# Performance work log

Hardware: AMD Instinct MI355X
Metric: run time of the kernel (lower is better)

## Reference

```python
import jax, jax.numpy as jnp
import numpy as np

K = 4
TEMPERATURE = 34.0
OUT_CH = 256
KSIZE = 3
PAD = 1


def setup_inputs() -> dict:
    key = jax.random.key(0)
    ks = jax.random.split(key, 6)
    B, C, H, W = 16, 256, 56, 56
    hidden = int(C * 0.25) + 1  # 65
    x = jax.random.normal(ks[0], (B, C, H, W), dtype=jnp.float32)
    w_fc1 = jax.random.normal(ks[1], (hidden, C), dtype=jnp.float32) * (2.0 / C) ** 0.5
    w_fc2 = jax.random.normal(ks[2], (K, hidden), dtype=jnp.float32) * (2.0 / hidden) ** 0.5
    b_fc2 = jnp.zeros((K,), dtype=jnp.float32)
    weight = jax.random.normal(ks[3], (OUT_CH, C, KSIZE, KSIZE), dtype=jnp.float32) * 0.05
    bias = jax.random.normal(ks[4], (K, OUT_CH), dtype=jnp.float32) * 0.01
    return {"x": x, "w_fc1": w_fc1, "w_fc2": w_fc2, "b_fc2": b_fc2,
            "weight": weight, "bias": bias}


def _attention(x, w_fc1, w_fc2, b_fc2):
    pooled = x.mean(axis=(2, 3))                     # [B, C] adaptive avgpool(1)
    h = jax.nn.relu(pooled @ w_fc1.T)                # 1x1 conv == linear
    raw = h @ w_fc2.T + b_fc2                        # [B, K]
    # gradient_approximation: hard one-hot fwd, softmax(x/T) bwd (straight-through)
    hard = jax.nn.one_hot(jnp.argmax(raw, axis=1), raw.shape[1], dtype=raw.dtype)
    soft = jax.nn.softmax(raw / TEMPERATURE, axis=1)
    att = jax.lax.stop_gradient(hard - soft) + soft
    return att, raw


def _quantize_banks(weight):
    # WDoReFaQuantizer with 'modified' scheme, bits 2..K+1, STE on the round step
    w = weight.reshape(-1)
    t = jnp.tanh(w)
    xq = t / jnp.max(jnp.abs(t))
    xq = (xq + 1.0) * 0.5                            # in [0, 1]
    banks = []
    for bit in range(2, 2 + K):
        a = float(1 << bit)
        q = jnp.minimum(jnp.floor(a * xq), a - 1.0) / a
        q = jax.lax.stop_gradient(q - xq) + xq       # STE: identity backward
        banks.append(q * 2.0 - 1.0)
    return jnp.stack(banks)                          # [K, O*C*k*k]


def reference(x, w_fc1, w_fc2, b_fc2, weight, bias):
    B, C, H, W = x.shape
    att, raw = _attention(x, w_fc1, w_fc2, b_fc2)    # [B, K], [B, K]
    wq = _quantize_banks(weight)                     # [K, N]
    agg_w = (att @ wq).reshape(B, OUT_CH, C, KSIZE, KSIZE)
    agg_b = att @ bias                               # [B, OUT_CH]

    def conv1(xi, wi):  # xi: [C,H,W], wi: [O,C,k,k]
        return jax.lax.conv_general_dilated(
            xi[None], wi, window_strides=(1, 1),
            padding=[(PAD, PAD), (PAD, PAD)],
            dimension_numbers=("NCHW", "OIHW", "NCHW"))[0]

    out = jax.vmap(conv1)(x, agg_w) + agg_b[:, :, None, None]
    return (out, raw)
```

## Files before the change

kernel.cpp:

```cpp
#include <hip/hip_runtime.h>
#include <math.h>

#define NB 16
#define NC 256
#define NH 56
#define NW 56
#define NHW 3136
#define NHID 65
#define NK 4
#define NOC 256
#define WN 589824
#define OUT0 12845056

#define WS_POOLED 0
#define WS_KB     4096
#define WS_MAX    4112
#define WS_MAXP   4128
#define WS_WQF    8192
#define WQB_OFF   32768ul
#define XP_OFF    4751360ul
#define WS_NEED   32325632ul

typedef unsigned int u32;
typedef unsigned short u16;
typedef unsigned long long u64;
typedef __attribute__((ext_vector_type(8))) short s8v;
typedef __attribute__((ext_vector_type(16))) float f16v;

__device__ __forceinline__ u16 f2bf(float f) {
    union { float f; u32 u; } v; v.f = f;
    u32 u = v.u;
    return (u16)((u + 0x7fffu + ((u >> 16) & 1u)) >> 16);
}

__device__ __forceinline__ void gload_lds16(const void* g, void* l) {
    __builtin_amdgcn_global_load_lds((const __attribute__((address_space(1))) u32*)g,
                                     (__attribute__((address_space(3))) u32*)l, 16, 0, 0);
}


__global__ __launch_bounds__(256) void k_prep(const float* __restrict__ x,
                                              const float* __restrict__ w,
                                              float* __restrict__ ws,
                                              float* __restrict__ scratch) {
    const int tid = threadIdx.x;
    if (blockIdx.x >= 896) {
        int j = blockIdx.x - 896;
        float m = 0.f;
        for (int i = j * 256 + tid; i < WN; i += 65536)
            m = fmaxf(m, fabsf(tanhf(w[i])));
        for (int off = 32; off > 0; off >>= 1) m = fmaxf(m, __shfl_down(m, off, 64));
        __shared__ float part[4];
        int lane = tid & 63, wv = tid >> 6;
        if (lane == 0) part[wv] = m;
        __syncthreads();
        if (tid == 0)
            ws[WS_MAXP + j] = fmaxf(fmaxf(part[0], part[1]), fmaxf(part[2], part[3]));
        return;
    }
    const int by = blockIdx.x;
    const int b = by / 56, y = by % 56;
    const int c16 = tid >> 4, q = tid & 15;
    __shared__ __align__(8) u16 Lbt[56 * 264];
    __shared__ float pl[256];
    u16* xp = (u16*)((char*)ws + XP_OFF);

    #pragma unroll
    for (int ci = 0; ci < 16; ++ci) {
        int c = ci * 16 + c16;
        float4 v = make_float4(0.f, 0.f, 0.f, 0.f);
        if (q < 14) {
            v = *(const float4*)(x + ((size_t)(b * 256 + c)) * NHW + (size_t)y * 56 + q * 4);
            Lbt[(q * 4 + 0) * 264 + c] = f2bf(v.x);
            Lbt[(q * 4 + 1) * 264 + c] = f2bf(v.y);
            Lbt[(q * 4 + 2) * 264 + c] = f2bf(v.z);
            Lbt[(q * 4 + 3) * 264 + c] = f2bf(v.w);
        }
        float s = v.x + v.y + v.z + v.w;
        s += __shfl_down(s, 8, 16);
        s += __shfl_down(s, 4, 16);
        s += __shfl_down(s, 2, 16);
        s += __shfl_down(s, 1, 16);
        if (q == 0) pl[c] = s;
    }
    __syncthreads();
    scratch[(size_t)by * 256 + tid] = pl[tid];
    u64* rowp = (u64*)xp + (size_t)(b * 58 + y + 1) * (58 * 64);
    for (int idx = tid; idx < 58 * 64; idx += 256) {
        int col = idx >> 6, cp = idx & 63;
        u64 v = 0ull;
        if (col >= 1 && col <= 56)
            v = *(const u64*)(Lbt + (col - 1) * 264 + cp * 4);
        rowp[idx] = v;
    }
    if (y == 0 || y == 55) {
        int row = (y == 0) ? 0 : 57;
        u64* brow = (u64*)xp + (size_t)(b * 58 + row) * (58 * 64);
        for (int idx = tid; idx < 58 * 64; idx += 256) brow[idx] = 0ull;
    }
}

__global__ __launch_bounds__(256) void k_mid(const float* __restrict__ w_fc1,
                                             const float* __restrict__ w_fc2,
                                             const float* __restrict__ b_fc2,
                                             const float* __restrict__ w,
                                             float* __restrict__ ws,
                                             const float* __restrict__ scratch,
                                             float* __restrict__ out_raw) {
    const int tid = threadIdx.x;
    if (blockIdx.x < 16) {
        const int b = blockIdx.x;
        __shared__ float pl[NC];
        __shared__ float hs[NHID];
        __shared__ float raws[NK];
        float p = 0.f;
        for (int y = 0; y < 56; ++y)
            p += scratch[((size_t)(b * 56 + y)) * 256 + tid];
        pl[tid] = p * (1.0f / NHW);
        __syncthreads();
        if (tid < NHID) {
            float s = 0.f;
            for (int c = 0; c < NC; ++c) s = fmaf(pl[c], w_fc1[tid * NC + c], s);
            hs[tid] = fmaxf(s, 0.f);
        }
        __syncthreads();
        if (tid < NK) {
            float s = b_fc2[tid];
            for (int j = 0; j < NHID; ++j) s = fmaf(hs[j], w_fc2[tid * NHID + j], s);
            raws[tid] = s;
            out_raw[b * NK + tid] = s;
        }
        __syncthreads();
        if (tid == 0) {
            int best = 0;
            for (int k = 1; k < NK; ++k) if (raws[k] > raws[best]) best = k;
            ((int*)(ws + WS_KB))[b] = best;
        }
        return;
    }
    __shared__ float mred[4];
    float mv = ws[WS_MAXP + tid];
    for (int off = 32; off > 0; off >>= 1) mv = fmaxf(mv, __shfl_down(mv, off, 64));
    if ((tid & 63) == 0) mred[tid >> 6] = mv;
    __syncthreads();
    const float maxt = fmaxf(fmaxf(mred[0], mred[1]), fmaxf(mred[2], mred[3]));

    u16* wqp = (u16*)((char*)ws + WQB_OFF);
    int idx = (blockIdx.x - 16) * 256 + tid;
    int o = idx >> 7, c2 = idx & 127;
    int ch0 = c2 * 2;
    int cs = ch0 >> 5, cc = ch0 & 31;
    int ks2 = cc >> 4, hf = (cc >> 3) & 1, j = cc & 7;
    int n = o & 31, ot = o >> 5;
    const float* wp = w + ((size_t)o * 256 + ch0) * 9;
    float t0[9], t1[9];
    #pragma unroll
    for (int t = 0; t < 9; ++t) t0[t] = tanhf(wp[t]);
    #pragma unroll
    for (int t = 0; t < 9; ++t) t1[t] = tanhf(wp[9 + t]);
    #pragma unroll
    for (int bank = 0; bank < 4; ++bank) {
        float a = (float)(4 << bank);
        #pragma unroll
        for (int tap = 0; tap < 9; ++tap) {
            float xq0 = (t0[tap] / maxt + 1.f) * 0.5f;
            float xq1 = (t1[tap] / maxt + 1.f) * 0.5f;
            float q0 = fminf(floorf(a * xq0), a - 1.f) / a * 2.f - 1.f;
            float q1 = fminf(floorf(a * xq1), a - 1.f) / a * 2.f - 1.f;
            u32 pk = (u32)f2bf(q0) | ((u32)f2bf(q1) << 16);
            size_t off16 = ((((size_t)((bank * 8 + ot) * 8 + cs)) * 18 + tap * 2 + ks2) * 64
                            + hf * 32 + n) * 8 + j;
            *(u32*)(wqp + off16) = pk;
        }
    }
}

__global__ __launch_bounds__(512, 4) void k_conv_mfma(const float* __restrict__ bias,
                                                      const float* __restrict__ ws_f,
                                                      float* __restrict__ out) {
    const int L = blockIdx.x;
    const int xcd = L & 7, slot = L >> 3;
    const int oq = slot >> 4;
    const int pair = xcd * 16 + (slot & 15);
    const int b = pair >> 3, strip = pair & 7;
    const int r0 = strip * 7;
    const int tid = threadIdx.x;
    const int wv = tid >> 6, lane = tid & 63;
    const int n = lane & 31, hf = lane >> 5;
    const int vw = (wv + (slot & 7)) & 7;
    const int ntile = (vw < 5) ? 2 : 1;
    const int t0 = (vw < 5) ? vw * 2 : 10 + (vw - 5);
    const int kb = ((const int*)(ws_f + WS_KB))[b];
    const u16* wqp = (const u16*)((const char*)ws_f + WQB_OFF);
    const u16* xp  = (const u16*)((const char*)ws_f + XP_OFF);

    __shared__ __align__(16) u16 Xl[2][9216];
    __shared__ __align__(16) u16 Al[2][9216];

    int bofs[2];
    #pragma unroll
    for (int t = 0; t < 2; ++t) {
        int p = (t0 + t) * 32 + n;
        if (t >= ntile || p > 391) p = 391;
        int pr = p / 56, pc = p - pr * 56;
        bofs[t] = pr * 2048 + hf * 1024 + pc * 16;
    }
    const int colc = (lane < 58) ? lane : 57;
    const u16* xsrc = xp + (((size_t)(b * 58 + r0)) * 58 + colc) * 256;
    const u16* ab0 = wqp + (size_t)((kb * 8 + oq * 2 + 0) * 8) * (18 * 64 * 8);
    const u16* ab1 = wqp + (size_t)((kb * 8 + oq * 2 + 1) * 8) * (18 * 64 * 8);

    f16v acc0[2], acc1[2];
    #pragma unroll
    for (int t = 0; t < 2; ++t) { acc0[t] = (f16v)0.f; acc1[t] = (f16v)0.f; }

    const int sbase = (wv < 4) ? wv * 5 : 20 + (wv - 4) * 4;
    const int scnt  = (wv < 4) ? 5 : 4;
#define STAGE(stn, bn)                                                                   \
    {                                                                                    \
        const int csn = (stn) >> 1, ksn = (stn) & 1;                                     \
        _Pragma("unroll")                                                                \
        for (int i = 0; i < 5; ++i)                                                      \
            if (i < scnt) {                                                              \
                int seg = sbase + i;                                                     \
                if (seg < 18) {                                                          \
                    gload_lds16(xsrc + (size_t)(seg >> 1) * (58 * 256) + (stn) * 16 + (seg & 1) * 8, \
                                (void*)(&Xl[bn][seg * 512]));                            \
                } else {                                                                 \
                    int aa = seg - 18;                                                   \
                    int tile = (aa >= 9) ? 1 : 0;                                        \
                    int tap = aa - tile * 9;                                             \
                    const u16* ab = tile ? ab1 : ab0;                                    \
                    gload_lds16(ab + (size_t)(csn * 18 + tap * 2 + ksn) * 512 + lane * 8, \
                                (void*)(&Al[bn][aa * 512]));                             \
                }                                                                        \
            }                                                                            \
    }

    STAGE(0, 0);

    #pragma unroll 1
    for (int st = 0; st < 16; ++st) {
        int pb = st & 1;
        if (st < 15) {
            STAGE(st + 1, pb ^ 1);
            if (wv < 4) { asm volatile("s_waitcnt vmcnt(5)" ::: "memory"); }
            else        { asm volatile("s_waitcnt vmcnt(4)" ::: "memory"); }
        } else {
            asm volatile("s_waitcnt vmcnt(0)" ::: "memory");
        }
        __builtin_amdgcn_s_barrier();
        __builtin_amdgcn_s_setprio(1);
        const u16* AB = &Al[pb][0];
        const char* XB = (const char*)&Xl[pb][0];
        #pragma unroll
        for (int tap = 0; tap < 9; ++tap) {
            s8v a0 = *(const s8v*)(AB + tap * 512 + lane * 8);
            s8v a1 = *(const s8v*)(AB + (9 + tap) * 512 + lane * 8);
            const int r = tap / 3, s = tap % 3;
            const int coff = r * 2048 + s * 16;
            #pragma unroll
            for (int t = 0; t < 2; ++t)
                if (t < ntile) {
                    s8v bf = *(const s8v*)(XB + bofs[t] + coff);
                    acc0[t] = __builtin_amdgcn_mfma_f32_32x32x16_bf16(a0, bf, acc0[t], 0, 0, 0);
                    acc1[t] = __builtin_amdgcn_mfma_f32_32x32x16_bf16(a1, bf, acc1[t], 0, 0, 0);
                }
        }
        __builtin_amdgcn_s_setprio(0);
        asm volatile("" ::: "memory");
        __builtin_amdgcn_s_barrier();
    }
#undef STAGE

    #pragma unroll
    for (int t = 0; t < 2; ++t)
        if (t < ntile) {
            int p = (t0 + t) * 32 + n;
            if (p < 392) {
                int pr = p / 56, pc = p - pr * 56;
                float* op = out + (size_t)b * 256 * NHW + (size_t)(r0 + pr) * 56 + pc;
                #pragma unroll
                for (int reg = 0; reg < 16; ++reg) {
                    int m = (reg & 3) + 8 * (reg >> 2) + 4 * hf;
                    int o0 = oq * 64 + m;
                    op[(size_t)o0 * NHW] = acc0[t][reg] + bias[kb * NOC + o0];
                    op[(size_t)(o0 + 32) * NHW] = acc1[t][reg] + bias[kb * NOC + o0 + 32];
                }
            }
        }
}


__global__ __launch_bounds__(256) void k_pool(const float* __restrict__ x,
                                              float* __restrict__ ws) {
    int plane = blockIdx.x;
    const float* p = x + (size_t)plane * NHW;
    float s = 0.f;
    for (int i = threadIdx.x; i < NHW; i += 256) s += p[i];
    for (int off = 32; off > 0; off >>= 1) s += __shfl_down(s, off, 64);
    __shared__ float part[4];
    int lane = threadIdx.x & 63, wv = threadIdx.x >> 6;
    if (lane == 0) part[wv] = s;
    __syncthreads();
    if (threadIdx.x == 0)
        ws[WS_POOLED + plane] = part[0] + part[1] + part[2] + part[3];
}

__global__ __launch_bounds__(256) void k_fc(const float* __restrict__ w_fc1,
                                            const float* __restrict__ w_fc2,
                                            const float* __restrict__ b_fc2,
                                            float* __restrict__ ws,
                                            float* __restrict__ out_raw) {
    __shared__ float pl[NB * NC];
    __shared__ float hs[NB][NHID];
    __shared__ float raws[NB][NK];
    for (int i = threadIdx.x; i < NB * NC; i += 256)
        pl[i] = ws[WS_POOLED + i] * (1.0f / NHW);
    __syncthreads();
    for (int idx = threadIdx.x; idx < NB * NHID; idx += 256) {
        int b = idx / NHID, j = idx % NHID;
        float s = 0.f;
        for (int c = 0; c < NC; ++c) s = fmaf(pl[b * NC + c], w_fc1[j * NC + c], s);
        hs[b][j] = fmaxf(s, 0.f);
    }
    __syncthreads();
    if (threadIdx.x < NB * NK) {
        int b = threadIdx.x / NK, k = threadIdx.x % NK;
        float s = b_fc2[k];
        for (int j = 0; j < NHID; ++j) s = fmaf(hs[b][j], w_fc2[k * NHID + j], s);
        raws[b][k] = s;
        out_raw[b * NK + k] = s;
    }
    __syncthreads();
    if (threadIdx.x < NB) {
        int best = 0;
        for (int k = 1; k < NK; ++k)
            if (raws[threadIdx.x][k] > raws[threadIdx.x][best]) best = k;
        ((int*)(ws + WS_KB))[threadIdx.x] = best;
    }
}

__global__ __launch_bounds__(256) void k_maxtanh(const float* __restrict__ w,
                                                 float* __restrict__ ws) {
    float m = 0.f;
    for (int i = blockIdx.x * 256 + threadIdx.x; i < WN; i += gridDim.x * 256)
        m = fmaxf(m, fabsf(tanhf(w[i])));
    for (int off = 32; off > 0; off >>= 1) m = fmaxf(m, __shfl_down(m, off, 64));
    __shared__ float part[4];
    int lane = threadIdx.x & 63, wv = threadIdx.x >> 6;
    if (lane == 0) part[wv] = m;
    __syncthreads();
    if (threadIdx.x == 0) {
        float t = fmaxf(fmaxf(part[0], part[1]), fmaxf(part[2], part[3]));
        atomicMax((unsigned int*)ws + WS_MAX, __float_as_uint(t));
    }
}

__global__ __launch_bounds__(256) void k_quant(const float* __restrict__ w,
                                               float* __restrict__ ws) {
    float maxt = __uint_as_float(((const unsigned int*)ws)[WS_MAX]);
    float* wqf = ws + WS_WQF;
    for (int i = blockIdx.x * 256 + threadIdx.x; i < WN; i += gridDim.x * 256) {
        float t = tanhf(w[i]);
        float xq = (t / maxt + 1.0f) * 0.5f;
        #pragma unroll
        for (int k = 0; k < NK; ++k) {
            float a = (float)(4 << k);
            float q = fminf(floorf(a * xq), a - 1.0f) / a;
            wqf[(size_t)k * WN + i] = q * 2.0f - 1.0f;
        }
    }
}

__global__ __launch_bounds__(256) void k_conv(const float* __restrict__ x,
                                              const float* __restrict__ bias,
                                              const float* __restrict__ ws,
                                              float* __restrict__ out) {
    const int o_base = blockIdx.x * 16;
    const int row_base = blockIdx.y * 7;
    const int b = blockIdx.z;
    const int tid = threadIdx.x;
    const int w = tid & 63;
    const int og = tid >> 6;
    const int wc = (w < 56) ? w : 55;
    const int kb = ((const int*)(ws + WS_KB))[b];
    const float* wqf = ws + WS_WQF + (size_t)kb * WN;

    __shared__ float Xl[8][9][58];
    __shared__ float Wl[16][72];

    float acc[4][7];
    #pragma unroll
    for (int i = 0; i < 4; ++i)
        #pragma unroll
        for (int j = 0; j < 7; ++j) acc[i][j] = 0.f;

    for (int c0 = 0; c0 < NC; c0 += 8) {
        for (int idx = tid; idx < 1152; idx += 256) {
            int o = idx / 72, rem = idx - o * 72;
            Wl[o][rem] = wqf[(size_t)(o_base + o) * 2304 + c0 * 9 + rem];
        }
        for (int idx = tid; idx < 4176; idx += 256) {
            int c = idx / 522, rem = idx - c * 522;
            int ly = rem / 58, lx = rem - ly * 58;
            int gy = row_base - 1 + ly, gx = lx - 1;
            float v = 0.f;
            if (gy >= 0 && gy < NH && (unsigned)gx < (unsigned)NW)
                v = x[(((size_t)b * NC + c0 + c) * NH + gy) * NW + gx];
            Xl[c][ly][lx] = v;
        }
        __syncthreads();
        #pragma unroll 1
        for (int c = 0; c < 8; ++c) {
            float xv[9][3];
            #pragma unroll
            for (int ly = 0; ly < 9; ++ly)
                #pragma unroll
                for (int s = 0; s < 3; ++s)
                    xv[ly][s] = Xl[c][ly][wc + s];
            float wvv[4][9];
            #pragma unroll
            for (int i = 0; i < 4; ++i)
                #pragma unroll
                for (int t = 0; t < 9; ++t)
                    wvv[i][t] = Wl[og * 4 + i][c * 9 + t];
            #pragma unroll
            for (int i = 0; i < 4; ++i)
                #pragma unroll
                for (int j = 0; j < 7; ++j)
                    #pragma unroll
                    for (int r = 0; r < 3; ++r)
                        #pragma unroll
                        for (int s = 0; s < 3; ++s)
                            acc[i][j] = fmaf(wvv[i][r * 3 + s], xv[j + r][s], acc[i][j]);
        }
        __syncthreads();
    }

    if (w < 56) {
        #pragma unroll
        for (int i = 0; i < 4; ++i) {
            int o = o_base + og * 4 + i;
            float bb = bias[kb * NOC + o];
            #pragma unroll
            for (int j = 0; j < 7; ++j)
                out[(((size_t)b * NOC + o) * NH + (row_base + j)) * NW + w] = acc[i][j] + bb;
        }
    }
}

extern "C" void kernel_launch(void* const* d_in, const int* in_sizes, int n_in,
                              void* d_out, int out_size, void* d_ws, size_t ws_size,
                              hipStream_t stream) {
    const float* x      = (const float*)d_in[0];
    const float* w_fc1  = (const float*)d_in[1];
    const float* w_fc2  = (const float*)d_in[2];
    const float* b_fc2  = (const float*)d_in[3];
    const float* weight = (const float*)d_in[4];
    const float* bias   = (const float*)d_in[5];
    float* out = (float*)d_out;
    float* ws  = (float*)d_ws;

    if (ws_size >= WS_NEED) {
        hipLaunchKernelGGL(k_prep, dim3(1152), dim3(256), 0, stream, x, weight, ws, out);
        hipLaunchKernelGGL(k_mid, dim3(144), dim3(256), 0, stream,
                           w_fc1, w_fc2, b_fc2, weight, ws, out, out + OUT0);
        hipLaunchKernelGGL(k_conv_mfma, dim3(512), dim3(512), 0, stream, bias, ws, out);
    } else {
        hipLaunchKernelGGL(k_pool, dim3(NB * NC), dim3(256), 0, stream, x, ws);
        hipLaunchKernelGGL(k_fc, dim3(1), dim3(256), 0, stream,
                           w_fc1, w_fc2, b_fc2, ws, out + OUT0);
        hipLaunchKernelGGL(k_maxtanh, dim3(256), dim3(256), 0, stream, weight, ws);
        hipLaunchKernelGGL(k_quant, dim3(512), dim3(256), 0, stream, weight, ws);
        hipLaunchKernelGGL(k_conv, dim3(16, 8, NB), dim3(256), 0, stream, x, bias, ws, out);
    }
}
```

Measured before the change: 186.6 us.

## Reorder padded bf16 input into channel-slab rows with XOR-swizzled LDS columns

The prep kernel now writes the bf16 input as per-16-channel slabs, one contiguous 1920-byte row per (slab, batch, y), with the two 8-channel halves of each column placed at an XOR-swizzled offset. Top and bottom halo rows are no longer stored; the conv kernel points those loads at a small shared zero slab instead. Each row is fetched as contiguous 16-byte chunks straight into LDS, and B-fragment reads use the swizzled offsets. The aim is fewer LDS bank conflicts and more contiguous global loads, at the cost of three precomputed offsets per tile and a changed workspace layout that the producer and consumer must agree on.

```diff
diff --git a/kernel.cpp b/kernel.cpp
--- a/kernel.cpp
+++ b/kernel.cpp
@@ -17,6 +17,7 @@
 #define WS_MAX    4112
 #define WS_MAXP   4128
 #define WS_WQF    8192
+#define ZSL_OFF   24576ul
 #define WQB_OFF   32768ul
 #define XP_OFF    4751360ul
 #define WS_NEED   32325632ul
@@ -36,6 +37,10 @@
 __device__ __forceinline__ void gload_lds16(const void* g, void* l) {
     __builtin_amdgcn_global_load_lds((const __attribute__((address_space(1))) u32*)g,
                                      (__attribute__((address_space(3))) u32*)l, 16, 0, 0);
+}
+
+__device__ __forceinline__ int xswz(int col, int hf) {
+    return (col * 32 + hf * 16) ^ (((col >> 2) & 7) << 4);
 }
 
 
@@ -61,9 +66,8 @@
     const int by = blockIdx.x;
     const int b = by / 56, y = by % 56;
     const int c16 = tid >> 4, q = tid & 15;
-    __shared__ __align__(8) u16 Lbt[56 * 264];
+    __shared__ __align__(16) u16 Lbt[56 * 264];
     __shared__ float pl[256];
-    u16* xp = (u16*)((char*)ws + XP_OFF);
 
     #pragma unroll
     for (int ci = 0; ci < 16; ++ci) {
@@ -85,18 +89,20 @@
     }
     __syncthreads();
     scratch[(size_t)by * 256 + tid] = pl[tid];
-    u64* rowp = (u64*)xp + (size_t)(b * 58 + y + 1) * (58 * 64);
-    for (int idx = tid; idx < 58 * 64; idx += 256) {
-        int col = idx >> 6, cp = idx & 63;
-        u64 v = 0ull;
+
+    char* xpn = (char*)ws + XP_OFF;
+    #pragma unroll 1
+    for (int g = tid; g < 16 * 58 * 2; g += 256) {
+        int cs = g / 116, rm = g - cs * 116;
+        int col = rm >> 1, hf = rm & 1;
+        s8v v = (s8v)0;
         if (col >= 1 && col <= 56)
-            v = *(const u64*)(Lbt + (col - 1) * 264 + cp * 4);
-        rowp[idx] = v;
-    }
-    if (y == 0 || y == 55) {
-        int row = (y == 0) ? 0 : 57;
-        u64* brow = (u64*)xp + (size_t)(b * 58 + row) * (58 * 64);
-        for (int idx = tid; idx < 58 * 64; idx += 256) brow[idx] = 0ull;
+            v = *(const s8v*)(Lbt + (col - 1) * 264 + cs * 16 + hf * 8);
+        *(s8v*)(xpn + (((size_t)cs * 16 + b) * 56 + y) * 1920 + xswz(col, hf)) = v;
+    }
+    if (by == 0) {
+        u64* z = (u64*)((char*)ws + ZSL_OFF);
+        for (int i = tid; i < 240; i += 256) z[i] = 0ull;
     }
 }
 
@@ -192,21 +198,22 @@
     const int t0 = (vw < 5) ? vw * 2 : 10 + (vw - 5);
     const int kb = ((const int*)(ws_f + WS_KB))[b];
     const u16* wqp = (const u16*)((const char*)ws_f + WQB_OFF);
-    const u16* xp  = (const u16*)((const char*)ws_f + XP_OFF);
+    const char* xpn = (const char*)ws_f + XP_OFF;
+    const char* zsl = (const char*)ws_f + ZSL_OFF;
 
     __shared__ __align__(16) u16 Xl[2][9216];
     __shared__ __align__(16) u16 Al[2][9216];
 
-    int bofs[2];
+    int bofs[2][3];
     #pragma unroll
     for (int t = 0; t < 2; ++t) {
         int p = (t0 + t) * 32 + n;
         if (t >= ntile || p > 391) p = 391;
         int pr = p / 56, pc = p - pr * 56;
-        bofs[t] = pr * 2048 + hf * 1024 + pc * 16;
-    }
-    const int colc = (lane < 58) ? lane : 57;
-    const u16* xsrc = xp + (((size_t)(b * 58 + r0)) * 58 + colc) * 256;
+        #pragma unroll
+        for (int s = 0; s < 3; ++s)
+            bofs[t][s] = pr * 2048 + xswz(pc + s, hf);
+    }
     const u16* ab0 = wqp + (size_t)((kb * 8 + oq * 2 + 0) * 8) * (18 * 64 * 8);
     const u16* ab1 = wqp + (size_t)((kb * 8 + oq * 2 + 1) * 8) * (18 * 64 * 8);
 
@@ -224,8 +231,13 @@
             if (i < scnt) {                                                              \
                 int seg = sbase + i;                                                     \
                 if (seg < 18) {                                                          \
-                    gload_lds16(xsrc + (size_t)(seg >> 1) * (58 * 256) + (stn) * 16 + (seg & 1) * 8, \
-                                (void*)(&Xl[bn][seg * 512]));                            \
+                    int row = seg >> 1, half = seg & 1;                                  \
+                    int rr = r0 + row;                                                   \
+                    const char* src = (rr >= 1 && rr <= 56)                              \
+                        ? xpn + (((size_t)(stn) * 16 + b) * 56 + (rr - 1)) * 1920        \
+                        : zsl;                                                           \
+                    gload_lds16(src + half * 896 + lane * 16,                            \
+                                (void*)(&Xl[bn][row * 1024 + half * 448]));              \
                 } else {                                                                 \
                     int aa = seg - 18;                                                   \
                     int tile = (aa >= 9) ? 1 : 0;                                        \
@@ -258,11 +270,11 @@
             s8v a0 = *(const s8v*)(AB + tap * 512 + lane * 8);
             s8v a1 = *(const s8v*)(AB + (9 + tap) * 512 + lane * 8);
             const int r = tap / 3, s = tap % 3;
-            const int coff = r * 2048 + s * 16;
+            const int coff = r * 2048;
             #pragma unroll
             for (int t = 0; t < 2; ++t)
                 if (t < ntile) {
-                    s8v bf = *(const s8v*)(XB + bofs[t] + coff);
+                    s8v bf = *(const s8v*)(XB + bofs[t][s] + coff);
                     acc0[t] = __builtin_amdgcn_mfma_f32_32x32x16_bf16(a0, bf, acc0[t], 0, 0, 0);
                     acc1[t] = __builtin_amdgcn_mfma_f32_32x32x16_bf16(a1, bf, acc1[t], 0, 0, 0);
                 }
```

Measured after the change: 182.9 us. 2.0% less time.
